# Optimization experiments

Hardware: AMD Instinct MI355X
Metric: run time of the kernel (lower is better)

## Reference

```python
import jax, jax.numpy as jnp
import numpy as np

D = 1024
H = 16
DH = D // H  # 64
SCALE = DH ** (-0.5)

def setup_inputs() -> dict:
    key = jax.random.key(0)
    k1, k2, k3, k4, k5 = jax.random.split(key, 5)
    x = jax.random.normal(k1, (4, 2048, D), dtype=jnp.float32)
    w_qkv = jax.random.normal(k2, (D, 3 * D), dtype=jnp.float32) * (D ** -0.5)
    b_qkv = jax.random.normal(k3, (3 * D,), dtype=jnp.float32) * 0.02
    w_out = jax.random.normal(k4, (D, D), dtype=jnp.float32) * (D ** -0.5)
    b_out = jax.random.normal(k5, (D,), dtype=jnp.float32) * 0.02
    return {"x": x, "w_qkv": w_qkv, "b_qkv": b_qkv, "w_out": w_out, "b_out": b_out}

def reference(x, w_qkv, b_qkv, w_out, b_out):
    B, S, C = x.shape
    qkv = x @ w_qkv + b_qkv                          # [B,S,3D]
    qkv = qkv.reshape(B, S, 3, H, DH)
    qkv = jnp.transpose(qkv, (0, 3, 2, 1, 4))        # [B,H,3,S,DH]
    q, k, v = qkv[:, :, 0], qkv[:, :, 1], qkv[:, :, 2]
    q = q * SCALE
    scores = jnp.einsum('bhqd,bhkd->bhqk', q, k)     # [B,H,S,S]
    attn = jax.nn.softmax(scores.astype(jnp.float32), axis=-1).astype(scores.dtype)
    out = jnp.einsum('bhqk,bhkd->bhqd', attn, v)     # [B,H,S,DH]
    out = jnp.transpose(out, (0, 2, 1, 3)).reshape(B, S, C)
    return out @ w_out + b_out
```

## Files before the change

kernel.cpp:

```cpp
#include <hip/hip_runtime.h>

#define D_ 1024
#define H_ 16
#define DH_ 64
#define S_ 2048
#define B_ 4
#define N_ (B_*S_)
#define M3_ 3072
#define QSC_ 0.18033688011112042f

typedef _Float16 f16;
typedef _Float16 f16x8 __attribute__((ext_vector_type(8)));
typedef _Float16 f16x4 __attribute__((ext_vector_type(4)));
typedef _Float16 f16x2 __attribute__((ext_vector_type(2)));
typedef __fp16   h16x2 __attribute__((ext_vector_type(2)));
typedef float    f32x4 __attribute__((ext_vector_type(4)));

typedef __attribute__((address_space(1))) void gvoid;
typedef __attribute__((address_space(3))) void lvoid;

__device__ __forceinline__ void gl16(const f16* g, f16* l) {
    __builtin_amdgcn_global_load_lds((gvoid*)g, (lvoid*)l, 16, 0, 0);
}

__device__ __forceinline__ f16x2 pk_cvt(float a, float b) {
#if __has_builtin(__builtin_amdgcn_cvt_pkrtz)
    h16x2 t = __builtin_amdgcn_cvt_pkrtz(a, b);
    return __builtin_bit_cast(f16x2, t);
#else
    f16x2 r; r[0] = (f16)a; r[1] = (f16)b; return r;
#endif
}

__global__ __launch_bounds__(256) void cvt_x_kernel(const float* __restrict__ in,
                                                    f16* __restrict__ out) {
    size_t i = ((size_t)blockIdx.x * 256 + threadIdx.x) * 4;
    float4 f = *reinterpret_cast<const float4*>(in + i);
    f16x4 o;
    o[0] = (f16)f.x; o[1] = (f16)f.y; o[2] = (f16)f.z; o[3] = (f16)f.w;
    *reinterpret_cast<f16x4*>(out + i) = o;
}

__global__ __launch_bounds__(256) void wt_cvt_kernel(const float* __restrict__ in,
                                                     f16* __restrict__ out,
                                                     int K, int Nc) {
    __shared__ float tile[32][33];
    int tx = threadIdx.x & 31, ty = threadIdx.x >> 5;
    int c = blockIdx.x * 32 + tx;
    #pragma unroll
    for (int i = 0; i < 4; i++) {
        int r = blockIdx.y * 32 + ty + i * 8;
        tile[ty + i * 8][tx] = in[(size_t)r * Nc + c];
    }
    __syncthreads();
    #pragma unroll
    for (int i = 0; i < 4; i++) {
        int r2 = blockIdx.x * 32 + ty + i * 8;
        int c2 = blockIdx.y * 32 + tx;
        out[(size_t)r2 * K + c2] = (f16)tile[tx][ty + i * 8];
    }
}

__global__ __launch_bounds__(256) void gemm_qkv_kernel(
        const f16* __restrict__ A, const f16* __restrict__ Bt,
        const float* __restrict__ bias,
        f16* __restrict__ qo, f16* __restrict__ ko, f16* __restrict__ vTo) {
    __shared__ __align__(16) f16 As[128 * 32];
    __shared__ __align__(16) f16 Bs[128 * 32];
    const int tid  = threadIdx.x;
    const int lane = tid & 63, w = tid >> 6;
    const int quad = lane >> 4, lrow = lane & 15;
    const int wm = (w & 1) * 64, wn = (w >> 1) * 64;
    const int n0 = blockIdx.x * 128, m0 = blockIdx.y * 128;

    f32x4 acc[4][4];
    #pragma unroll
    for (int i = 0; i < 4; i++)
        #pragma unroll
        for (int j = 0; j < 4; j++) acc[i][j] = {0.f, 0.f, 0.f, 0.f};

    const int ar0 = tid >> 2, ap0 = tid & 3;
    const f16* Ag0 = A  + (size_t)(n0 + ar0) * D_ + ap0 * 8;
    const f16* Ag1 = Ag0 + (size_t)64 * D_;
    const f16* Bg0 = Bt + (size_t)(m0 + ar0) * D_ + ap0 * 8;
    const f16* Bg1 = Bg0 + (size_t)64 * D_;
    f16* Asl = As + tid * 8;
    f16* Bsl = Bs + tid * 8;

    for (int kt = 0; kt < D_ / 32; kt++) {
        gl16(Ag0 + kt * 32, Asl);
        gl16(Ag1 + kt * 32, Asl + 64 * 32);
        gl16(Bg0 + kt * 32, Bsl);
        gl16(Bg1 + kt * 32, Bsl + 64 * 32);
        __syncthreads();
        f16x8 af[4], bf[4];
        #pragma unroll
        for (int i = 0; i < 4; i++)
            af[i] = *reinterpret_cast<const f16x8*>(&As[(wm + i * 16 + lrow) * 32 + quad * 8]);
        #pragma unroll
        for (int j = 0; j < 4; j++)
            bf[j] = *reinterpret_cast<const f16x8*>(&Bs[(wn + j * 16 + lrow) * 32 + quad * 8]);
        #pragma unroll
        for (int i = 0; i < 4; i++)
            #pragma unroll
            for (int j = 0; j < 4; j++)
                acc[i][j] = __builtin_amdgcn_mfma_f32_16x16x32_f16(af[i], bf[j], acc[i][j], 0, 0, 0);
        __syncthreads();
    }

    #pragma unroll
    for (int j = 0; j < 4; j++) {
        int m   = m0 + wn + j * 16 + lrow;
        int sec = m >> 10;
        int hd  = m & 1023;
        int hh  = hd >> 6, d = hd & 63;
        float bb = bias[m];
        if (sec == 2) {
            #pragma unroll
            for (int i = 0; i < 4; i++) {
                int n = n0 + wm + i * 16 + quad * 4;
                int bidx = n >> 11, s = n & 2047;
                f16x4 o;
                #pragma unroll
                for (int r = 0; r < 4; r++) o[r] = (f16)(acc[i][j][r] + bb);
                *reinterpret_cast<f16x4*>(
                    &vTo[(((size_t)(bidx * H_ + hh)) * DH_ + d) * S_ + s]) = o;
            }
        } else {
            f16* dst = (sec == 0) ? qo : ko;
            float sc = (sec == 0) ? QSC_ : 1.0f;
            #pragma unroll
            for (int i = 0; i < 4; i++) {
                #pragma unroll
                for (int r = 0; r < 4; r++) {
                    int n = n0 + wm + i * 16 + quad * 4 + r;
                    int bidx = n >> 11, s = n & 2047;
                    dst[(((size_t)(bidx * H_ + hh)) * S_ + s) * DH_ + d] =
                        (f16)((acc[i][j][r] + bb) * sc);
                }
            }
        }
    }
}

__global__ __launch_bounds__(256) void attn_kernel(
        const f16* __restrict__ q, const f16* __restrict__ k,
        const f16* __restrict__ vT, f16* __restrict__ ctx) {
    __shared__ __align__(16) f16 Ks[2][128 * 72];
    __shared__ __align__(16) f16 Vs[2][64 * 136];
    const int tid  = threadIdx.x;
    const int lane = tid & 63, w = tid >> 6;
    const int quad = lane >> 4, lrow = lane & 15;
    const int id = blockIdx.x;
    const int bh = id & 63;
    const int q0 = (id >> 6) * 256;
    const int b  = bh >> 4, h = bh & 15;
    const f16* qb = q  + (size_t)bh * S_ * DH_;
    const f16* kb = k  + (size_t)bh * S_ * DH_;
    const f16* vb = vT + (size_t)bh * DH_ * S_;

    f16x8 qf[4][2];
    #pragma unroll
    for (int f = 0; f < 4; f++)
        #pragma unroll
        for (int hf = 0; hf < 2; hf++)
            qf[f][hf] = *reinterpret_cast<const f16x8*>(
                qb + (size_t)(q0 + w * 64 + f * 16 + lrow) * DH_ + hf * 32 + quad * 8);

    f16x8 ones8;
    #pragma unroll
    for (int i = 0; i < 8; i++) ones8[i] = (f16)1.f;

    f32x4 lacc[4];
    f32x4 ot[4][4];
    #pragma unroll
    for (int f = 0; f < 4; f++) {
        lacc[f] = {0.f, 0.f, 0.f, 0.f};
        #pragma unroll
        for (int dj = 0; dj < 4; dj++) ot[f][dj] = {0.f, 0.f, 0.f, 0.f};
    }

    int kslot[4], kpart[4], vrow[4], vpart[4];
    #pragma unroll
    for (int i = 0; i < 4; i++) {
        int ch = tid + i * 256;
        int g = ch >> 3, jj = g & 7, qd = (g >> 3) & 3;
        kslot[i] = (g & ~31) + ((jj >> 2) << 4) + (qd << 2) + (jj & 3);
        kpart[i] = ch & 7;
        vrow[i] = ch >> 4; vpart[i] = ch & 15;
    }

    f16x8 krg[4], vrg[4];
    #pragma unroll
    for (int i = 0; i < 4; i++) {
        int ch = tid + i * 256;
        krg[i] = *reinterpret_cast<const f16x8*>(kb + (size_t)(ch >> 3) * DH_ + (ch & 7) * 8);
        vrg[i] = *reinterpret_cast<const f16x8*>(vb + (size_t)vrow[i] * S_ + vpart[i] * 8);
    }
    #pragma unroll
    for (int i = 0; i < 4; i++) {
        *reinterpret_cast<f16x8*>(&Ks[0][kslot[i] * 72 + kpart[i] * 8]) = krg[i];
        *reinterpret_cast<f16x8*>(&Vs[0][vrow[i] * 136 + vpart[i] * 8]) = vrg[i];
    }
    #pragma unroll
    for (int i = 0; i < 4; i++) {
        int ch = tid + i * 256;
        krg[i] = *reinterpret_cast<const f16x8*>(kb + (size_t)(128 + (ch >> 3)) * DH_ + (ch & 7) * 8);
        vrg[i] = *reinterpret_cast<const f16x8*>(vb + (size_t)vrow[i] * S_ + 128 + vpart[i] * 8);
    }
    __syncthreads();

    const int NT = S_ / 128;
    for (int kt = 0; kt < NT; kt++) {
        const int cur = kt & 1;
        const f16* Kc = Ks[cur];
        const f16* Vc = Vs[cur];

        #pragma unroll
        for (int t = 0; t < 4; t++) {
            f16x8 p8[4];
            #pragma unroll
            for (int half = 0; half < 2; half++) {
                int mb = 2 * t + half;
                f16x8 kf0 = *reinterpret_cast<const f16x8*>(&Kc[(mb * 16 + lrow) * 72 + quad * 8]);
                f16x8 kf1 = *reinterpret_cast<const f16x8*>(&Kc[(mb * 16 + lrow) * 72 + 32 + quad * 8]);
                #pragma unroll
                for (int f = 0; f < 4; f++) {
                    f32x4 st = {0.f, 0.f, 0.f, 0.f};
                    st = __builtin_amdgcn_mfma_f32_16x16x32_f16(kf0, qf[f][0], st, 0, 0, 0);
                    st = __builtin_amdgcn_mfma_f32_16x16x32_f16(kf1, qf[f][1], st, 0, 0, 0);
                    f16x2 lo = pk_cvt(__builtin_amdgcn_exp2f(st[0]),
                                      __builtin_amdgcn_exp2f(st[1]));
                    f16x2 hi = pk_cvt(__builtin_amdgcn_exp2f(st[2]),
                                      __builtin_amdgcn_exp2f(st[3]));
                    p8[f][half * 4 + 0] = lo[0]; p8[f][half * 4 + 1] = lo[1];
                    p8[f][half * 4 + 2] = hi[0]; p8[f][half * 4 + 3] = hi[1];
                }
            }
            #pragma unroll
            for (int dj = 0; dj < 4; dj++) {
                f16x8 vf = *reinterpret_cast<const f16x8*>(
                    &Vc[(dj * 16 + lrow) * 136 + t * 32 + quad * 8]);
                #pragma unroll
                for (int f = 0; f < 4; f++)
                    ot[f][dj] = __builtin_amdgcn_mfma_f32_16x16x32_f16(vf, p8[f], ot[f][dj], 0, 0, 0);
            }
            #pragma unroll
            for (int f = 0; f < 4; f++)
                lacc[f] = __builtin_amdgcn_mfma_f32_16x16x32_f16(ones8, p8[f], lacc[f], 0, 0, 0);
        }

        if (kt + 1 < NT) {
            const int nxt = cur ^ 1;
            #pragma unroll
            for (int i = 0; i < 4; i++) {
                *reinterpret_cast<f16x8*>(&Ks[nxt][kslot[i] * 72 + kpart[i] * 8]) = krg[i];
                *reinterpret_cast<f16x8*>(&Vs[nxt][vrow[i] * 136 + vpart[i] * 8]) = vrg[i];
            }
            if (kt + 2 < NT) {
                const int kv2 = (kt + 2) * 128;
                #pragma unroll
                for (int i = 0; i < 4; i++) {
                    int ch = tid + i * 256;
                    krg[i] = *reinterpret_cast<const f16x8*>(kb + (size_t)(kv2 + (ch >> 3)) * DH_ + (ch & 7) * 8);
                    vrg[i] = *reinterpret_cast<const f16x8*>(vb + (size_t)vrow[i] * S_ + kv2 + vpart[i] * 8);
                }
            }
            __syncthreads();
        }
    }

    #pragma unroll
    for (int f = 0; f < 4; f++) {
        float inv = 1.0f / lacc[f][0];
        int qrow = q0 + w * 64 + f * 16 + lrow;
        #pragma unroll
        for (int dj = 0; dj < 4; dj++) {
            f16x4 o;
            #pragma unroll
            for (int r = 0; r < 4; r++) o[r] = (f16)(ot[f][dj][r] * inv);
            *reinterpret_cast<f16x4*>(
                &ctx[((size_t)(b * S_ + qrow)) * D_ + h * DH_ + dj * 16 + quad * 4]) = o;
        }
    }
}

__global__ __launch_bounds__(256) void gemm_out_kernel(
        const f16* __restrict__ A, const f16* __restrict__ Bt,
        const float* __restrict__ bias, float* __restrict__ out) {
    __shared__ __align__(16) f16 As[128 * 32];
    __shared__ __align__(16) f16 Bs[128 * 32];
    const int tid  = threadIdx.x;
    const int lane = tid & 63, w = tid >> 6;
    const int quad = lane >> 4, lrow = lane & 15;
    const int wm = (w & 1) * 64, wn = (w >> 1) * 64;
    const int n0 = blockIdx.x * 128, m0 = blockIdx.y * 128;

    f32x4 acc[4][4];
    #pragma unroll
    for (int i = 0; i < 4; i++)
        #pragma unroll
        for (int j = 0; j < 4; j++) acc[i][j] = {0.f, 0.f, 0.f, 0.f};

    const int ar0 = tid >> 2, ap0 = tid & 3;
    const f16* Ag0 = A  + (size_t)(n0 + ar0) * D_ + ap0 * 8;
    const f16* Ag1 = Ag0 + (size_t)64 * D_;
    const f16* Bg0 = Bt + (size_t)(m0 + ar0) * D_ + ap0 * 8;
    const f16* Bg1 = Bg0 + (size_t)64 * D_;
    f16* Asl = As + tid * 8;
    f16* Bsl = Bs + tid * 8;

    for (int kt = 0; kt < D_ / 32; kt++) {
        gl16(Ag0 + kt * 32, Asl);
        gl16(Ag1 + kt * 32, Asl + 64 * 32);
        gl16(Bg0 + kt * 32, Bsl);
        gl16(Bg1 + kt * 32, Bsl + 64 * 32);
        __syncthreads();
        f16x8 af[4], bf[4];
        #pragma unroll
        for (int i = 0; i < 4; i++)
            af[i] = *reinterpret_cast<const f16x8*>(&As[(wm + i * 16 + lrow) * 32 + quad * 8]);
        #pragma unroll
        for (int j = 0; j < 4; j++)
            bf[j] = *reinterpret_cast<const f16x8*>(&Bs[(wn + j * 16 + lrow) * 32 + quad * 8]);
        #pragma unroll
        for (int i = 0; i < 4; i++)
            #pragma unroll
            for (int j = 0; j < 4; j++)
                acc[i][j] = __builtin_amdgcn_mfma_f32_16x16x32_f16(af[i], bf[j], acc[i][j], 0, 0, 0);
        __syncthreads();
    }

    #pragma unroll
    for (int j = 0; j < 4; j++) {
        int m = m0 + wn + j * 16 + lrow;
        float bb = bias[m];
        #pragma unroll
        for (int i = 0; i < 4; i++)
            #pragma unroll
            for (int r = 0; r < 4; r++) {
                int n = n0 + wm + i * 16 + quad * 4 + r;
                out[(size_t)n * D_ + m] = acc[i][j][r] + bb;
            }
    }
}

extern "C" void kernel_launch(void* const* d_in, const int* in_sizes, int n_in,
                              void* d_out, int out_size, void* d_ws, size_t ws_size,
                              hipStream_t stream) {
    (void)in_sizes; (void)n_in; (void)out_size; (void)ws_size;
    const float* x     = (const float*)d_in[0];
    const float* w_qkv = (const float*)d_in[1];
    const float* b_qkv = (const float*)d_in[2];
    const float* w_out = (const float*)d_in[3];
    const float* b_out = (const float*)d_in[4];
    float* out = (float*)d_out;

    char* ws = (char*)d_ws;
    const size_t MB = 1024 * 1024;
    f16* xb    = (f16*)(ws);
    f16* wqkvT = (f16*)(ws + 16 * MB);
    f16* woutT = (f16*)(ws + 22 * MB);
    f16* qs    = (f16*)(ws + 24 * MB);
    f16* kk    = (f16*)(ws + 40 * MB);
    f16* vTb   = (f16*)(ws + 72 * MB);
    f16* ctx   = xb;

    cvt_x_kernel<<<(N_ * D_) / (256 * 4), 256, 0, stream>>>(x, xb);
    wt_cvt_kernel<<<dim3(M3_ / 32, D_ / 32), 256, 0, stream>>>(w_qkv, wqkvT, D_, M3_);
    wt_cvt_kernel<<<dim3(D_ / 32, D_ / 32), 256, 0, stream>>>(w_out, woutT, D_, D_);
    gemm_qkv_kernel<<<dim3(N_ / 128, M3_ / 128), 256, 0, stream>>>(xb, wqkvT, b_qkv, qs, kk, vTb);
    attn_kernel<<<(B_ * H_) * (S_ / 256), 256, 0, stream>>>(qs, kk, vTb, ctx);
    gemm_out_kernel<<<dim3(N_ / 128, D_ / 128), 256, 0, stream>>>(ctx, woutT, b_out, out);
}
```

Baseline: 284.2 us.

## Restructure attention: async K loads to swizzled LDS, V read from global, smaller q tile

The attention kernel now stages only K in LDS, filling it through asynchronous global_load_lds into an XOR-swizzled unpadded layout. V fragments are read straight from global memory instead of through a shared buffer. The query tile per block drops from 256 to 128 rows, doubling the grid, and launch bounds request 4 blocks per CU to raise occupancy. This removes the register-staged prefetch and V shared-memory traffic, but it adds direct global V loads inside the inner loop, which depend on L2/cache hits, and it halves reuse of each K tile.

```diff
diff --git a/kernel.cpp b/kernel.cpp
--- a/kernel.cpp
+++ b/kernel.cpp
@@ -143,89 +143,86 @@
     }
 }
 
-__global__ __launch_bounds__(256) void attn_kernel(
+__global__ __launch_bounds__(256, 4) void attn_kernel(
         const f16* __restrict__ q, const f16* __restrict__ k,
         const f16* __restrict__ vT, f16* __restrict__ ctx) {
-    __shared__ __align__(16) f16 Ks[2][128 * 72];
-    __shared__ __align__(16) f16 Vs[2][64 * 136];
+    __shared__ __align__(16) f16 Ks[2][128 * 64];
     const int tid  = threadIdx.x;
     const int lane = tid & 63, w = tid >> 6;
     const int quad = lane >> 4, lrow = lane & 15;
     const int id = blockIdx.x;
     const int bh = id & 63;
-    const int q0 = (id >> 6) * 256;
+    const int q0 = (id >> 6) * 128;
     const int b  = bh >> 4, h = bh & 15;
     const f16* qb = q  + (size_t)bh * S_ * DH_;
     const f16* kb = k  + (size_t)bh * S_ * DH_;
     const f16* vb = vT + (size_t)bh * DH_ * S_;
 
-    f16x8 qf[4][2];
-    #pragma unroll
-    for (int f = 0; f < 4; f++)
+    f16x8 qf[2][2];
+    #pragma unroll
+    for (int f = 0; f < 2; f++)
         #pragma unroll
         for (int hf = 0; hf < 2; hf++)
             qf[f][hf] = *reinterpret_cast<const f16x8*>(
-                qb + (size_t)(q0 + w * 64 + f * 16 + lrow) * DH_ + hf * 32 + quad * 8);
+                qb + (size_t)(q0 + w * 32 + f * 16 + lrow) * DH_ + hf * 32 + quad * 8);
 
     f16x8 ones8;
     #pragma unroll
     for (int i = 0; i < 8; i++) ones8[i] = (f16)1.f;
 
-    f32x4 lacc[4];
-    f32x4 ot[4][4];
-    #pragma unroll
-    for (int f = 0; f < 4; f++) {
+    f32x4 lacc[2];
+    f32x4 ot[2][4];
+    #pragma unroll
+    for (int f = 0; f < 2; f++) {
         lacc[f] = {0.f, 0.f, 0.f, 0.f};
         #pragma unroll
         for (int dj = 0; dj < 4; dj++) ot[f][dj] = {0.f, 0.f, 0.f, 0.f};
     }
 
-    int kslot[4], kpart[4], vrow[4], vpart[4];
+    int koff[4];
     #pragma unroll
     for (int i = 0; i < 4; i++) {
-        int ch = tid + i * 256;
-        int g = ch >> 3, jj = g & 7, qd = (g >> 3) & 3;
-        kslot[i] = (g & ~31) + ((jj >> 2) << 4) + (qd << 2) + (jj & 3);
-        kpart[i] = ch & 7;
-        vrow[i] = ch >> 4; vpart[i] = ch & 15;
-    }
-
-    f16x8 krg[4], vrg[4];
-    #pragma unroll
-    for (int i = 0; i < 4; i++) {
-        int ch = tid + i * 256;
-        krg[i] = *reinterpret_cast<const f16x8*>(kb + (size_t)(ch >> 3) * DH_ + (ch & 7) * 8);
-        vrg[i] = *reinterpret_cast<const f16x8*>(vb + (size_t)vrow[i] * S_ + vpart[i] * 8);
-    }
-    #pragma unroll
-    for (int i = 0; i < 4; i++) {
-        *reinterpret_cast<f16x8*>(&Ks[0][kslot[i] * 72 + kpart[i] * 8]) = krg[i];
-        *reinterpret_cast<f16x8*>(&Vs[0][vrow[i] * 136 + vpart[i] * 8]) = vrg[i];
-    }
-    #pragma unroll
-    for (int i = 0; i < 4; i++) {
-        int ch = tid + i * 256;
-        krg[i] = *reinterpret_cast<const f16x8*>(kb + (size_t)(128 + (ch >> 3)) * DH_ + (ch & 7) * 8);
-        vrg[i] = *reinterpret_cast<const f16x8*>(vb + (size_t)vrow[i] * S_ + 128 + vpart[i] * 8);
-    }
+        int c = i * 256 + tid;
+        int s = c >> 3, p = c & 7;
+        int g = (s & ~31) | (((s >> 2) & 3) << 3) | (((s >> 4) & 1) << 2) | (s & 3);
+        koff[i] = g * DH_ + ((p ^ (s & 7)) * 8);
+    }
+
+    #pragma unroll
+    for (int i = 0; i < 4; i++)
+        gl16(kb + koff[i], &Ks[0][(i * 256 + tid) * 8]);
     __syncthreads();
+
+    const int xr0 = (quad ^ (lrow & 7)) * 8;
+    const int xr1 = ((quad + 4) ^ (lrow & 7)) * 8;
 
     const int NT = S_ / 128;
     for (int kt = 0; kt < NT; kt++) {
         const int cur = kt & 1;
         const f16* Kc = Ks[cur];
-        const f16* Vc = Vs[cur];
+        const int kv0 = kt * 128;
 
         #pragma unroll
         for (int t = 0; t < 4; t++) {
-            f16x8 p8[4];
+            f16x8 vf[4];
+            #pragma unroll
+            for (int dj = 0; dj < 4; dj++)
+                vf[dj] = *reinterpret_cast<const f16x8*>(
+                    vb + (size_t)(dj * 16 + lrow) * S_ + kv0 + t * 32 + quad * 8);
+            if (t == 0 && kt + 1 < NT) {
+                #pragma unroll
+                for (int i = 0; i < 4; i++)
+                    gl16(kb + (size_t)(kv0 + 128) * DH_ + koff[i],
+                         &Ks[cur ^ 1][(i * 256 + tid) * 8]);
+            }
+            f16x8 p8[2];
             #pragma unroll
             for (int half = 0; half < 2; half++) {
-                int mb = 2 * t + half;
-                f16x8 kf0 = *reinterpret_cast<const f16x8*>(&Kc[(mb * 16 + lrow) * 72 + quad * 8]);
-                f16x8 kf1 = *reinterpret_cast<const f16x8*>(&Kc[(mb * 16 + lrow) * 72 + 32 + quad * 8]);
-                #pragma unroll
-                for (int f = 0; f < 4; f++) {
+                int rb = (2 * t + half) * 16 + lrow;
+                f16x8 kf0 = *reinterpret_cast<const f16x8*>(&Kc[rb * 64 + xr0]);
+                f16x8 kf1 = *reinterpret_cast<const f16x8*>(&Kc[rb * 64 + xr1]);
+                #pragma unroll
+                for (int f = 0; f < 2; f++) {
                     f32x4 st = {0.f, 0.f, 0.f, 0.f};
                     st = __builtin_amdgcn_mfma_f32_16x16x32_f16(kf0, qf[f][0], st, 0, 0, 0);
                     st = __builtin_amdgcn_mfma_f32_16x16x32_f16(kf1, qf[f][1], st, 0, 0, 0);
@@ -238,42 +235,21 @@
                 }
             }
             #pragma unroll
-            for (int dj = 0; dj < 4; dj++) {
-                f16x8 vf = *reinterpret_cast<const f16x8*>(
-                    &Vc[(dj * 16 + lrow) * 136 + t * 32 + quad * 8]);
-                #pragma unroll
-                for (int f = 0; f < 4; f++)
-                    ot[f][dj] = __builtin_amdgcn_mfma_f32_16x16x32_f16(vf, p8[f], ot[f][dj], 0, 0, 0);
-            }
-            #pragma unroll
-            for (int f = 0; f < 4; f++)
+            for (int dj = 0; dj < 4; dj++)
+                #pragma unroll
+                for (int f = 0; f < 2; f++)
+                    ot[f][dj] = __builtin_amdgcn_mfma_f32_16x16x32_f16(vf[dj], p8[f], ot[f][dj], 0, 0, 0);
+            #pragma unroll
+            for (int f = 0; f < 2; f++)
                 lacc[f] = __builtin_amdgcn_mfma_f32_16x16x32_f16(ones8, p8[f], lacc[f], 0, 0, 0);
         }
-
-        if (kt + 1 < NT) {
-            const int nxt = cur ^ 1;
-            #pragma unroll
-            for (int i = 0; i < 4; i++) {
-                *reinterpret_cast<f16x8*>(&Ks[nxt][kslot[i] * 72 + kpart[i] * 8]) = krg[i];
-                *reinterpret_cast<f16x8*>(&Vs[nxt][vrow[i] * 136 + vpart[i] * 8]) = vrg[i];
-            }
-            if (kt + 2 < NT) {
-                const int kv2 = (kt + 2) * 128;
-                #pragma unroll
-                for (int i = 0; i < 4; i++) {
-                    int ch = tid + i * 256;
-                    krg[i] = *reinterpret_cast<const f16x8*>(kb + (size_t)(kv2 + (ch >> 3)) * DH_ + (ch & 7) * 8);
-                    vrg[i] = *reinterpret_cast<const f16x8*>(vb + (size_t)vrow[i] * S_ + kv2 + vpart[i] * 8);
-                }
-            }
-            __syncthreads();
-        }
-    }
-
-    #pragma unroll
-    for (int f = 0; f < 4; f++) {
+        __syncthreads();
+    }
+
+    #pragma unroll
+    for (int f = 0; f < 2; f++) {
         float inv = 1.0f / lacc[f][0];
-        int qrow = q0 + w * 64 + f * 16 + lrow;
+        int qrow = q0 + w * 32 + f * 16 + lrow;
         #pragma unroll
         for (int dj = 0; dj < 4; dj++) {
             f16x4 o;
@@ -370,6 +346,6 @@
     wt_cvt_kernel<<<dim3(M3_ / 32, D_ / 32), 256, 0, stream>>>(w_qkv, wqkvT, D_, M3_);
     wt_cvt_kernel<<<dim3(D_ / 32, D_ / 32), 256, 0, stream>>>(w_out, woutT, D_, D_);
     gemm_qkv_kernel<<<dim3(N_ / 128, M3_ / 128), 256, 0, stream>>>(xb, wqkvT, b_qkv, qs, kk, vTb);
-    attn_kernel<<<(B_ * H_) * (S_ / 256), 256, 0, stream>>>(qs, kk, vTb, ctx);
+    attn_kernel<<<(B_ * H_) * (S_ / 128), 256, 0, stream>>>(qs, kk, vTb, ctx);
     gemm_out_kernel<<<dim3(N_ / 128, D_ / 128), 256, 0, stream>>>(ctx, woutT, b_out, out);
 }
```

Result: slower. 331.0 us (+16.5%).
